# Optimization experiments

Hardware: AMD Instinct MI355X
Metric: run time of the kernel (lower is better)

The kernel has to match this reference:

```python
import jax, jax.numpy as jnp
import numpy as np

B, S, D, H, HD = 8, 1374, 384, 6, 64
NUM_PATCHES = 1369  # (518 // 14) ** 2
NUM_PREFIX = 5      # 1 cls + 4 registers


def setup_inputs() -> dict:
    key = jax.random.key(0)
    ks = jax.random.split(key, 10)
    init = 0.02  # truncated_normal(0.02) approximated by scaled normal
    x = jax.random.normal(ks[0], (B, S, D), jnp.float32)
    wq = jax.random.truncated_normal(ks[1], -2.0, 2.0, (D, H, HD), jnp.float32) * init
    wk = jax.random.truncated_normal(ks[2], -2.0, 2.0, (D, H, HD), jnp.float32) * init
    wv = jax.random.truncated_normal(ks[3], -2.0, 2.0, (D, H, HD), jnp.float32) * init
    wo = jax.random.truncated_normal(ks[4], -2.0, 2.0, (H, HD, D), jnp.float32) * init
    bq = jnp.zeros((H, HD), jnp.float32)
    bk = jnp.zeros((H, HD), jnp.float32)
    bv = jnp.zeros((H, HD), jnp.float32)
    bo = jnp.zeros((D,), jnp.float32)
    keep_patch_indices = jax.random.randint(ks[5], (B, NUM_PATCHES), 0, NUM_PATCHES).astype(jnp.int64)
    return {"x": x, "wq": wq, "bq": bq, "wk": wk, "bk": bk, "wv": wv, "bv": bv,
            "wo": wo, "bo": bo, "keep_patch_indices": keep_patch_indices, "k_patches": 685}


def reference(x, wq, bq, wk, bk, wv, bv, wo, bo, keep_patch_indices, k_patches):
    # q/k/v projections: DenseGeneral to (heads, head_dim)
    q = jnp.einsum('bsd,dhe->bshe', x, wq) + bq
    k = jnp.einsum('bsd,dhe->bshe', x, wk) + bk
    v = jnp.einsum('bsd,dhe->bshe', x, wv) + bv

    z = jnp.einsum('bqhd,bkhd->bhqk', q / (HD ** 0.5), k)  # [B,H,S,S]
    attn_logits = z  # saved BEFORE masking (used by 'mse' criterion)

    # dynamic scatter mask: patch columns >= k_patches get -inf
    num_selected = keep_patch_indices.shape[1]
    patch_idx = jnp.arange(num_selected)
    indices_to_mask = jnp.where(patch_idx >= k_patches, patch_idx, num_selected) + NUM_PREFIX
    # out-of-bounds indices (== num_selected + NUM_PREFIX) are dropped by JAX scatter semantics
    z = z.at[:, :, :, indices_to_mask].set(-jnp.inf)

    attn_map = jax.nn.softmax(z, axis=-1)
    zo = jnp.einsum('bhqk,bkhd->bqhd', attn_map, v)
    output = jnp.einsum('bqhd,hdo->bqo', zo, wo) + bo  # wo contracts (heads, head_dim)

    # attn_aggregate = ['cls_token','reg_token','patch_token'], zoom_map_criterion='mse'
    am = attn_logits.mean(axis=1)  # mean over heads -> [B,S,S]
    aggs = jnp.stack([
        am[:, 0:1, :].mean(axis=1),      # cls token
        am[:, 1:5, :].mean(axis=1),      # register tokens
        am[:, 5:1374, :].mean(axis=1),   # patch tokens
    ], axis=1)                            # [B,3,S]
    attn_agg = aggs.mean(axis=1)          # [B,S]
    return output, attn_agg
```

## Files before the change

kernel.cpp:

```cpp
#include <hip/hip_runtime.h>
#include <stdint.h>

#define BB 8
#define SS 1374
#define DD 384
#define HH 6
#define HDIM 64
#define MROWS (BB*SS)
#define NPFX 5
#define SPAD 1376

typedef __attribute__((ext_vector_type(8))) short bf16x8;
typedef __attribute__((ext_vector_type(4))) float f32x4;
typedef __attribute__((ext_vector_type(2))) unsigned int u32x2;
typedef __attribute__((ext_vector_type(4))) unsigned int u32x4;
typedef u32x4 __attribute__((aligned(4))) u32x4_u;

__device__ __forceinline__ unsigned short f2bf(float f){
  union { float f; unsigned int u; } v; v.f = f;
  return (unsigned short)((v.u + 0x7FFFu + ((v.u >> 16) & 1u)) >> 16);
}
__device__ __forceinline__ float bf2f(unsigned short b){
  union { float f; unsigned int u; } v; v.u = ((unsigned int)b) << 16; return v.f;
}
__device__ __forceinline__ unsigned int pk_bf16(float a, float b){
#if __has_builtin(__builtin_amdgcn_cvt_pk_bf16_f32)
  typedef __attribute__((ext_vector_type(2))) __bf16 bfv2;
  bfv2 p = __builtin_amdgcn_cvt_pk_bf16_f32(a, b);
  union { bfv2 v; unsigned int u; } c; c.v = p; return c.u;
#else
  return (unsigned int)f2bf(a) | ((unsigned int)f2bf(b) << 16);
#endif
}

__global__ void k_prep_x(const float* __restrict__ x, unsigned short* __restrict__ xb,
                         float* __restrict__ xbar){
  int b = blockIdx.x / 43, ch = blockIdx.x % 43;
  int d = threadIdx.x;
  int s0 = ch*32, s1 = s0 + 32; if (s1 > SS) s1 = SS;
  float acc = 0.f;
  for (int s = s0; s < s1; ++s){
    float v = x[((size_t)b*SS + s)*DD + d];
    float w = (s == 0) ? (1.f/3.f) : (s < 5) ? (1.f/12.f) : (1.f/4107.f);
    acc += w * v;
    xb[((size_t)b*SS + s)*DD + d] = f2bf(v);
  }
  atomicAdd(&xbar[b*DD + d], acc);
}

__global__ void k_conv_w(const float* __restrict__ wq, const float* __restrict__ wk,
                         const float* __restrict__ wv, const float* __restrict__ wo,
                         unsigned short* __restrict__ wbT, unsigned short* __restrict__ woT){
  int i = blockIdx.x*blockDim.x + threadIdx.x;
  if (i < 1152*384){
    int n = i / 384, d = i % 384;
    const float* w = (n < 384) ? wq : (n < 768) ? wk : wv;
    wbT[i] = f2bf(w[(size_t)d*384 + (n % 384)]);
  } else if (i < 1152*384 + 384*384){
    int j = i - 1152*384;
    int n = j / 384, k = j % 384;
    woT[j] = f2bf(wo[(size_t)k*384 + n]);
  }
}

__global__ void k_qbar(const float* __restrict__ xbar, const float* __restrict__ wq,
                       const float* __restrict__ bq, float* __restrict__ qbar){
  __shared__ float xs[DD];
  int b = blockIdx.x, t = threadIdx.x;
  xs[t] = xbar[b*DD + t];
  __syncthreads();
  float acc = bq[t];
  for (int d = 0; d < DD; ++d) acc += xs[d]*wq[(size_t)d*384 + t];
  qbar[b*384 + t] = acc;
}

__global__ void k_agg(const float* __restrict__ qbar, const unsigned short* __restrict__ kg,
                      float* __restrict__ out_agg){
  __shared__ float qs[384];
  int b = blockIdx.x / 6, sb = blockIdx.x % 6;
  int t = threadIdx.x;
  for (int i = t; i < 384; i += 256) qs[i] = qbar[b*384 + i];
  __syncthreads();
  int s = sb*256 + t;
  if (s >= SS) return;
  float acc = 0.f;
  for (int h = 0; h < HH; ++h){
    const unsigned short* kr = kg + (((size_t)(b*HH + h))*SS + s)*64;
    const float* qh = qs + h*64;
    for (int c = 0; c < 8; ++c){
      u32x4 v = *(const u32x4*)(kr + c*8);
      #pragma unroll
      for (int j = 0; j < 4; ++j){
        unsigned int u = v[j];
        acc += qh[c*8 + 2*j]     * bf2f((unsigned short)(u & 0xFFFFu));
        acc += qh[c*8 + 2*j + 1] * bf2f((unsigned short)(u >> 16));
      }
    }
  }
  out_agg[b*SS + s] = acc * (1.f/48.f);
}

template<int MODE>
__global__ __launch_bounds__(256) void k_gemm(
    const unsigned short* __restrict__ A, const unsigned short* __restrict__ Bt,
    const float* __restrict__ b0, const float* __restrict__ b1, const float* __restrict__ b2,
    unsigned short* __restrict__ qg, unsigned short* __restrict__ kgp,
    unsigned short* __restrict__ vt, float* __restrict__ out)
{
  int mt = blockIdx.x % 86, nt = blockIdx.x / 86;
  const int t = threadIdx.x;
  const int w = t >> 6, lane = t & 63, quad = lane >> 4, l16 = lane & 15;
  const int wm = w >> 1, wn = w & 1;
  constexpr int SMEM_SH = (MODE==0) ? 13824 : 17408;
  __shared__ unsigned short smem[SMEM_SH];
  unsigned short* As = smem;
  unsigned short* Bs = smem + 9216;
  f32x4 acc[4][2];
  #pragma unroll
  for (int i=0;i<4;i++){ acc[i][0] = (f32x4){0,0,0,0}; acc[i][1] = (f32x4){0,0,0,0}; }
  const int m0 = mt*128, n0 = nt*64;

  const int ar = t >> 1, akb = (t & 1) * 32;
  int ga = m0 + ar; if (ga > MROWS-1) ga = MROWS-1;
  const unsigned short* ap = A + (size_t)ga*384 + akb;
  const int br = t >> 2, bkb = (t & 3) * 16;
  const unsigned short* bp = Bt + (size_t)(n0 + br)*384 + bkb;

  u32x4 ra[4], rb[2];
  #pragma unroll
  for (int i=0;i<4;i++) ra[i] = *(const u32x4*)(ap + i*8);
  rb[0] = *(const u32x4*)(bp); rb[1] = *(const u32x4*)(bp + 8);

  for (int kc = 0; kc < 6; ++kc){
    __syncthreads();
    #pragma unroll
    for (int i=0;i<4;i++) *(u32x4*)(As + ar*72 + akb + i*8) = ra[i];
    *(u32x4*)(Bs + br*72 + bkb)     = rb[0];
    *(u32x4*)(Bs + br*72 + bkb + 8) = rb[1];
    __syncthreads();
    if (kc + 1 < 6){
      int kn = (kc+1)*64;
      #pragma unroll
      for (int i=0;i<4;i++) ra[i] = *(const u32x4*)(ap + kn + i*8);
      rb[0] = *(const u32x4*)(bp + kn); rb[1] = *(const u32x4*)(bp + kn + 8);
    }
    #pragma unroll
    for (int kh = 0; kh < 2; ++kh){
      bf16x8 af[4], bfr[2];
      #pragma unroll
      for (int rf = 0; rf < 4; ++rf)
        af[rf] = *(const bf16x8*)(As + (wm*64 + rf*16 + l16)*72 + kh*32 + quad*8);
      #pragma unroll
      for (int cf = 0; cf < 2; ++cf)
        bfr[cf] = *(const bf16x8*)(Bs + (wn*32 + cf*16 + l16)*72 + kh*32 + quad*8);
      #pragma unroll
      for (int rf = 0; rf < 4; ++rf)
        #pragma unroll
        for (int cf = 0; cf < 2; ++cf)
          acc[rf][cf] = __builtin_amdgcn_mfma_f32_16x16x32_bf16(af[rf], bfr[cf], acc[rf][cf], 0,0,0);
    }
  }

  const int b0r = m0 / SS, s0r = m0 % SS;
  __syncthreads();
  if (MODE == 1){
    float* CsF = (float*)smem;
    #pragma unroll
    for (int cf = 0; cf < 2; ++cf){
      int e = wn*32 + cf*16 + l16;
      float bias = b0[n0 + e];
      #pragma unroll
      for (int rf = 0; rf < 4; ++rf){
        int rr = wm*64 + rf*16 + quad*4;
        #pragma unroll
        for (int r4 = 0; r4 < 4; ++r4)
          CsF[(rr + r4)*68 + e] = acc[rf][cf][r4] + bias;
      }
    }
    __syncthreads();
    #pragma unroll
    for (int p = 0; p < 8; ++p){
      int r = p*16 + (t >> 4), c = t & 15;
      int rr = m0 + r;
      if (rr < MROWS){
        f32x4 v = *(const f32x4*)(CsF + r*68 + c*4);
        *(f32x4*)(out + (size_t)rr*384 + n0 + c*4) = v;
      }
    }
  } else {
    const int mat = nt / 6, h = nt - mat*6;
    const float* bvp = (mat==0) ? b0 : (mat==1) ? b1 : b2;
    const float vsc = (mat==0) ? 0.125f : 1.f;
    if (mat < 2){
      unsigned short* Cs = As;
      unsigned short* dst = (mat==0) ? qg : kgp;
      #pragma unroll
      for (int cf = 0; cf < 2; ++cf){
        int e = wn*32 + cf*16 + l16;
        float bias = bvp[h*64 + e];
        #pragma unroll
        for (int rf = 0; rf < 4; ++rf){
          int rr = wm*64 + rf*16 + quad*4;
          #pragma unroll
          for (int r4 = 0; r4 < 4; ++r4)
            Cs[(rr + r4)*72 + e] = f2bf((acc[rf][cf][r4] + bias)*vsc);
        }
      }
      __syncthreads();
      #pragma unroll
      for (int p = 0; p < 4; ++p){
        int r = p*32 + (t >> 3), c = t & 7;
        int rr = m0 + r;
        if (rr < MROWS){
          int s = s0r + r, bb = b0r;
          if (s >= SS){ s -= SS; ++bb; }
          u32x4 v = *(const u32x4*)(Cs + r*72 + c*8);
          *(u32x4*)(dst + (((size_t)(bb*HH + h))*SS + s)*64 + c*8) = v;
        }
      }
    } else {
      unsigned short* CsV = As;
      #pragma unroll
      for (int cf = 0; cf < 2; ++cf){
        int e = wn*32 + cf*16 + l16;
        float bias = bvp[h*64 + e];
        #pragma unroll
        for (int rf = 0; rf < 4; ++rf){
          int rr = wm*64 + rf*16 + quad*4;
          #pragma unroll
          for (int p = 0; p < 2; ++p)
            *(unsigned int*)(CsV + e*136 + rr + p*2) =
                pk_bf16(acc[rf][cf][p*2] + bias, acc[rf][cf][p*2+1] + bias);
        }
      }
      __syncthreads();
      const bool nowrap = (s0r + 127 < SS) && (m0 + 127 < MROWS);
      if (nowrap){
        int e = t >> 2;
        unsigned short* vrow = vt + ((size_t)(b0r*HH + h)*64 + e)*SPAD + s0r;
        #pragma unroll
        for (int i = 0; i < 4; ++i){
          int c = (t & 3)*4 + i;
          u32x4 v = *(const u32x4*)(CsV + e*136 + c*8);
          *(u32x4_u*)(vrow + c*8) = v;
        }
      } else {
        for (int idx = t; idx < 64*64; idx += 256){
          int e = idx >> 6, sp = (idx & 63)*2;
          int rr = m0 + sp;
          if (rr < MROWS){
            int s = s0r + sp, bb = b0r;
            if (s >= SS){ s -= SS; ++bb; }
            *(unsigned int*)(vt + ((size_t)(bb*HH + h)*64 + e)*SPAD + s) =
                *(const unsigned int*)(CsV + e*136 + sp);
          }
        }
      }
    }
  }
}

#define KSTR 72
__global__ __launch_bounds__(128) void k_attn(
    const unsigned short* __restrict__ qg, const unsigned short* __restrict__ kg,
    const unsigned short* __restrict__ vt, unsigned short* __restrict__ zo,
    const int* __restrict__ kpat)
{
  const int QB = 43;
  int qb = blockIdx.x % QB, bh = blockIdx.x / QB;
  int t = threadIdx.x, w = t >> 6, lane = t & 63, quad = lane >> 4, l16 = lane & 15;
  int SK = NPFX + kpat[0]; if (SK > SS) SK = SS; if (SK < 1) SK = 1;
  int niter = (SK + 63) >> 6;
  __shared__ unsigned short Ks[64*KSTR];
  __shared__ unsigned short Vs[64*KSTR];
  __shared__ unsigned short Ps[2][16*KSTR];
  unsigned short* Pw = &Ps[w][0];
  int q0 = qb*32 + w*16;
  bf16x8 aq[2];
  {
    int qrow = q0 + l16; if (qrow > SS-1) qrow = SS-1;
    const unsigned short* p = qg + ((size_t)bh*SS + qrow)*64;
    aq[0] = *(const bf16x8*)(p + quad*8);
    aq[1] = *(const bf16x8*)(p + 32 + quad*8);
  }
  f32x4 o[4];
  #pragma unroll
  for (int i=0;i<4;i++) o[i] = (f32x4){0.f,0.f,0.f,0.f};
  float rsum[4] = {0.f,0.f,0.f,0.f};

  const int srow = t >> 1, shalf = (t & 1)*32;
  const unsigned short* kbase = kg + ((size_t)bh*SS)*64;
  const unsigned short* vbase = vt + ((size_t)bh*64)*SPAD;
  u32x4 rk[4], rv[4];
  #pragma unroll
  for (int i=0;i<4;i++){
    rk[i] = *(const u32x4*)(kbase + (size_t)srow*64 + shalf + i*8);
    rv[i] = *(const u32x4*)(vbase + (size_t)srow*SPAD + shalf + i*8);
  }

  for (int it = 0; it < niter; ++it){
    int k0 = it*64;
    __syncthreads();
    #pragma unroll
    for (int i=0;i<4;i++){
      *(u32x4*)(Ks + srow*KSTR + shalf + i*8) = rk[i];
      *(u32x4*)(Vs + srow*KSTR + shalf + i*8) = rv[i];
    }
    __syncthreads();
    if (it + 1 < niter){
      int kn = k0 + 64;
      #pragma unroll
      for (int i=0;i<4;i++){
        rk[i] = *(const u32x4*)(kbase + (size_t)(kn + srow)*64 + shalf + i*8);
        rv[i] = *(const u32x4*)(vbase + (size_t)srow*SPAD + kn + shalf + i*8);
      }
    }
    bool tail = (k0 + 64 > SK);
    #pragma unroll
    for (int ks = 0; ks < 2; ++ks){
      float pp[2][4];
      #pragma unroll
      for (int ns = 0; ns < 2; ++ns){
        f32x4 zf = (f32x4){0.f,0.f,0.f,0.f};
        #pragma unroll
        for (int ec = 0; ec < 2; ++ec){
          bf16x8 bkf = *(const bf16x8*)(Ks + (ks*32 + 2*l16 + ns)*KSTR + ec*32 + quad*8);
          zf = __builtin_amdgcn_mfma_f32_16x16x32_bf16(aq[ec], bkf, zf, 0,0,0);
        }
        bool valid = !tail || (k0 + ks*32 + 2*l16 + ns) < SK;
        #pragma unroll
        for (int rg = 0; rg < 4; ++rg) pp[ns][rg] = valid ? __expf(zf[rg]) : 0.f;
      }
      #pragma unroll
      for (int rg = 0; rg < 4; ++rg){
        rsum[rg] += pp[0][rg] + pp[1][rg];
        *(unsigned int*)(Pw + (quad*4 + rg)*KSTR + ks*32 + 2*l16) =
            pk_bf16(pp[0][rg], pp[1][rg]);
      }
    }
    #pragma unroll
    for (int kc = 0; kc < 2; ++kc){
      bf16x8 ap = *(const bf16x8*)(Pw + l16*KSTR + kc*32 + quad*8);
      #pragma unroll
      for (int nc = 0; nc < 4; ++nc){
        bf16x8 vf = *(const bf16x8*)(Vs + (nc*16 + l16)*KSTR + kc*32 + quad*8);
        o[nc] = __builtin_amdgcn_mfma_f32_16x16x32_bf16(ap, vf, o[nc], 0,0,0);
      }
    }
  }
  int b = bh / HH, h = bh - (bh/HH)*HH;
  #pragma unroll
  for (int rg = 0; rg < 4; ++rg){
    float s = rsum[rg];
    #pragma unroll
    for (int off = 8; off >= 1; off >>= 1) s += __shfl_xor(s, off);
    int q = q0 + quad*4 + rg;
    if (q >= SS) continue;
    float inv = 1.f / s;
    unsigned short* dst = zo + ((size_t)b*SS + q)*384 + h*64;
    #pragma unroll
    for (int nc = 0; nc < 4; ++nc) dst[nc*16 + l16] = f2bf(o[nc][rg]*inv);
  }
}

extern "C" void kernel_launch(void* const* d_in, const int* in_sizes, int n_in,
                              void* d_out, int out_size, void* d_ws, size_t ws_size,
                              hipStream_t stream){
  const float* x  = (const float*)d_in[0];
  const float* wq = (const float*)d_in[1];
  const float* bq = (const float*)d_in[2];
  const float* wk = (const float*)d_in[3];
  const float* bk = (const float*)d_in[4];
  const float* wv = (const float*)d_in[5];
  const float* bv = (const float*)d_in[6];
  const float* wo = (const float*)d_in[7];
  const float* bo = (const float*)d_in[8];
  const int* kpat = (const int*)d_in[10];
  float* out = (float*)d_out;
  float* out_agg = out + (size_t)MROWS*DD;

  char* ws = (char*)d_ws;
  unsigned short* xb  = (unsigned short*)(ws);
  unsigned short* wbT = (unsigned short*)(ws +  8441856);
  unsigned short* woT = (unsigned short*)(ws +  9326592);
  unsigned short* qg  = (unsigned short*)(ws +  9621504);
  unsigned short* kg  = (unsigned short*)(ws + 18063360);
  unsigned short* vt  = (unsigned short*)(ws + 26505216);
  unsigned short* zo  = (unsigned short*)(ws + 34959360);
  float* xbar         = (float*)(ws + 43401216);
  float* qbar         = (float*)(ws + 43413504);
  (void)in_sizes; (void)n_in; (void)out_size; (void)ws_size;

  hipMemsetAsync(xbar, 0, BB*DD*sizeof(float), stream);
  k_prep_x<<<BB*43, DD, 0, stream>>>(x, xb, xbar);
  k_conv_w<<<((1152*384 + 384*384) + 255)/256, 256, 0, stream>>>(wq, wk, wv, wo, wbT, woT);
  k_qbar<<<BB, DD, 0, stream>>>(xbar, wq, bq, qbar);
  k_gemm<0><<<86*18, 256, 0, stream>>>(xb, wbT, bq, bk, bv, qg, kg, vt, nullptr);
  k_attn<<<48*43, 128, 0, stream>>>(qg, kg, vt, zo, kpat);
  k_agg<<<BB*6, 256, 0, stream>>>(qbar, kg, out_agg);
  k_gemm<1><<<86*6, 256, 0, stream>>>(zo, woT, bo, nullptr, nullptr, nullptr, nullptr, nullptr, out);
}
```

Measured before the change: 191.6 us.

## Double-buffer K/V tiles in attention and widen blocks to four waves

The attention kernel now uses 256-thread blocks, each covering 64 query rows with four waves, so every K/V tile loaded into shared memory is reused by twice as many queries. K/V tiles are double-buffered in LDS. The next tile is fetched with inline-asm global loads, issued before the current tile's MFMA work, and written to the alternate buffer after an explicit vmcnt drain. This is meant to overlap global load latency with compute and halve the per-query K/V traffic and barrier count. In exchange it uses more LDS and has fewer blocks in the grid, and the inline asm hides the loads from compiler scheduling.

Measured after the change: 192.6 us. Within noise of the previous version (+0.6%).

```diff
diff --git a/kernel.cpp b/kernel.cpp
--- a/kernel.cpp
+++ b/kernel.cpp
@@ -31,6 +31,12 @@
 #else
   return (unsigned int)f2bf(a) | ((unsigned int)f2bf(b) << 16);
 #endif
+}
+__device__ __forceinline__ void gload16(u32x4 &d, const unsigned short* a){
+  asm volatile("global_load_dwordx4 %0, %1, off" : "=v"(d) : "v"(a));
+}
+__device__ __forceinline__ void vdrain(){
+  asm volatile("s_waitcnt vmcnt(0)" ::: "memory");
 }
 
 __global__ void k_prep_x(const float* __restrict__ x, unsigned short* __restrict__ xb,
@@ -261,21 +267,21 @@
 }
 
 #define KSTR 72
-__global__ __launch_bounds__(128) void k_attn(
+__global__ __launch_bounds__(256) void k_attn(
     const unsigned short* __restrict__ qg, const unsigned short* __restrict__ kg,
     const unsigned short* __restrict__ vt, unsigned short* __restrict__ zo,
     const int* __restrict__ kpat)
 {
-  const int QB = 43;
+  const int QB = 22;
   int qb = blockIdx.x % QB, bh = blockIdx.x / QB;
   int t = threadIdx.x, w = t >> 6, lane = t & 63, quad = lane >> 4, l16 = lane & 15;
   int SK = NPFX + kpat[0]; if (SK > SS) SK = SS; if (SK < 1) SK = 1;
   int niter = (SK + 63) >> 6;
-  __shared__ unsigned short Ks[64*KSTR];
-  __shared__ unsigned short Vs[64*KSTR];
-  __shared__ unsigned short Ps[2][16*KSTR];
+  __shared__ unsigned short Ks[2][64*KSTR];
+  __shared__ unsigned short Vs[2][64*KSTR];
+  __shared__ unsigned short Ps[4][16*KSTR];
   unsigned short* Pw = &Ps[w][0];
-  int q0 = qb*32 + w*16;
+  int q0 = qb*64 + w*16;
   bf16x8 aq[2];
   {
     int qrow = q0 + l16; if (qrow > SS-1) qrow = SS-1;
@@ -288,33 +294,31 @@
   for (int i=0;i<4;i++) o[i] = (f32x4){0.f,0.f,0.f,0.f};
   float rsum[4] = {0.f,0.f,0.f,0.f};
 
-  const int srow = t >> 1, shalf = (t & 1)*32;
-  const unsigned short* kbase = kg + ((size_t)bh*SS)*64;
-  const unsigned short* vbase = vt + ((size_t)bh*64)*SPAD;
-  u32x4 rk[4], rv[4];
-  #pragma unroll
-  for (int i=0;i<4;i++){
-    rk[i] = *(const u32x4*)(kbase + (size_t)srow*64 + shalf + i*8);
-    rv[i] = *(const u32x4*)(vbase + (size_t)srow*SPAD + shalf + i*8);
-  }
+  const int srow = t >> 2, sc = (t & 3)*16;
+  const unsigned short* kptr = kg + ((size_t)bh*SS + srow)*64 + sc;
+  const unsigned short* vptr = vt + ((size_t)bh*64 + srow)*SPAD + sc;
+  u32x4 rk0, rk1, rv0, rv1;
+  gload16(rk0, kptr); gload16(rk1, kptr + 8);
+  gload16(rv0, vptr); gload16(rv1, vptr + 8);
+  vdrain();
+  *(u32x4*)(Ks[0] + srow*KSTR + sc)     = rk0;
+  *(u32x4*)(Ks[0] + srow*KSTR + sc + 8) = rk1;
+  *(u32x4*)(Vs[0] + srow*KSTR + sc)     = rv0;
+  *(u32x4*)(Vs[0] + srow*KSTR + sc + 8) = rv1;
+  __syncthreads();
 
   for (int it = 0; it < niter; ++it){
-    int k0 = it*64;
-    __syncthreads();
-    #pragma unroll
-    for (int i=0;i<4;i++){
-      *(u32x4*)(Ks + srow*KSTR + shalf + i*8) = rk[i];
-      *(u32x4*)(Vs + srow*KSTR + shalf + i*8) = rv[i];
-    }
-    __syncthreads();
-    if (it + 1 < niter){
+    int k0 = it*64, cur = it & 1;
+    bool more = (it + 1 < niter);
+    if (more){
       int kn = k0 + 64;
-      #pragma unroll
-      for (int i=0;i<4;i++){
-        rk[i] = *(const u32x4*)(kbase + (size_t)(kn + srow)*64 + shalf + i*8);
-        rv[i] = *(const u32x4*)(vbase + (size_t)srow*SPAD + kn + shalf + i*8);
-      }
-    }
+      gload16(rk0, kptr + (size_t)kn*64);
+      gload16(rk1, kptr + (size_t)kn*64 + 8);
+      gload16(rv0, vptr + kn);
+      gload16(rv1, vptr + kn + 8);
+    }
+    const unsigned short* Kc = Ks[cur];
+    const unsigned short* Vc = Vs[cur];
     bool tail = (k0 + 64 > SK);
     #pragma unroll
     for (int ks = 0; ks < 2; ++ks){
@@ -324,7 +328,7 @@
         f32x4 zf = (f32x4){0.f,0.f,0.f,0.f};
         #pragma unroll
         for (int ec = 0; ec < 2; ++ec){
-          bf16x8 bkf = *(const bf16x8*)(Ks + (ks*32 + 2*l16 + ns)*KSTR + ec*32 + quad*8);
+          bf16x8 bkf = *(const bf16x8*)(Kc + (ks*32 + 2*l16 + ns)*KSTR + ec*32 + quad*8);
           zf = __builtin_amdgcn_mfma_f32_16x16x32_bf16(aq[ec], bkf, zf, 0,0,0);
         }
         bool valid = !tail || (k0 + ks*32 + 2*l16 + ns) < SK;
@@ -343,9 +347,18 @@
       bf16x8 ap = *(const bf16x8*)(Pw + l16*KSTR + kc*32 + quad*8);
       #pragma unroll
       for (int nc = 0; nc < 4; ++nc){
-        bf16x8 vf = *(const bf16x8*)(Vs + (nc*16 + l16)*KSTR + kc*32 + quad*8);
+        bf16x8 vf = *(const bf16x8*)(Vc + (nc*16 + l16)*KSTR + kc*32 + quad*8);
         o[nc] = __builtin_amdgcn_mfma_f32_16x16x32_bf16(ap, vf, o[nc], 0,0,0);
       }
+    }
+    if (more){
+      int nxt = cur ^ 1;
+      vdrain();
+      *(u32x4*)(Ks[nxt] + srow*KSTR + sc)     = rk0;
+      *(u32x4*)(Ks[nxt] + srow*KSTR + sc + 8) = rk1;
+      *(u32x4*)(Vs[nxt] + srow*KSTR + sc)     = rv0;
+      *(u32x4*)(Vs[nxt] + srow*KSTR + sc + 8) = rv1;
+      __syncthreads();
     }
   }
   int b = bh / HH, h = bh - (bh/HH)*HH;
@@ -396,7 +409,7 @@
   k_conv_w<<<((1152*384 + 384*384) + 255)/256, 256, 0, stream>>>(wq, wk, wv, wo, wbT, woT);
   k_qbar<<<BB, DD, 0, stream>>>(xbar, wq, bq, qbar);
   k_gemm<0><<<86*18, 256, 0, stream>>>(xb, wbT, bq, bk, bv, qg, kg, vt, nullptr);
-  k_attn<<<48*43, 128, 0, stream>>>(qg, kg, vt, zo, kpat);
+  k_attn<<<48*22, 256, 0, stream>>>(qg, kg, vt, zo, kpat);
   k_agg<<<BB*6, 256, 0, stream>>>(qbar, kg, out_agg);
   k_gemm<1><<<86*6, 256, 0, stream>>>(zo, woT, bo, nullptr, nullptr, nullptr, nullptr, nullptr, out);
 }
```
